# Kernel optimization log

Measured on AMD Instinct MI355X. Metric: run time of the kernel, lower is better.

## Reference

```python
import jax, jax.numpy as jnp
import numpy as np

B, T, D, E, K = 8, 4096, 1024, 64, 2


def setup_inputs() -> dict:
    key = jax.random.key(0)
    k1, k2, k3, k4 = jax.random.split(key, 4)
    return {
        "mh_output": jax.random.normal(k1, (B, T, D), dtype=jnp.float32),
        "W_route": jax.random.normal(k2, (D, E), dtype=jnp.float32) * (1.0 / np.sqrt(D)),
        "b_route": jnp.zeros((E,), dtype=jnp.float32),
        "W_noise": jax.random.normal(k3, (D, E), dtype=jnp.float32) * (1.0 / np.sqrt(D)),
        "b_noise": jnp.zeros((E,), dtype=jnp.float32),
        "noise_u": jax.random.uniform(k4, (B, T, E), dtype=jnp.float32),
        "top_k": K,
    }


def reference(mh_output, W_route, b_route, W_noise, b_noise, noise_u, top_k):
    # [B,T,D] @ [D,E] -> [B,T,E]
    logits = jnp.einsum("btd,de->bte", mh_output, W_route) + b_route
    noise_logits = jnp.einsum("btd,de->bte", mh_output, W_noise) + b_noise
    noisy_logits = logits + noise_u * jax.nn.softplus(noise_logits)
    # top-k over experts
    top_k_logits, indices = jax.lax.top_k(noisy_logits, top_k)  # [B,T,K]
    # scatter top-k values back into -inf canvas == mask non-topk to -inf
    mask = jax.nn.one_hot(indices, E, dtype=jnp.bool_).any(axis=-2)  # [B,T,E]
    sparse_logits = jnp.where(mask, noisy_logits, -jnp.inf)
    router_output = jax.nn.softmax(sparse_logits, axis=-1)
    return (router_output, indices)
```

## Files before the change

### kernel.cpp

```cpp
#include <hip/hip_runtime.h>
#include <math.h>

#define MROWS 32768
#define DDIM  1024
#define EDIM  64
#define NCH   64
#define TILEM 64

typedef _Float16 f16x8 __attribute__((ext_vector_type(8)));
typedef float    f32x16 __attribute__((ext_vector_type(16)));

__global__ __launch_bounds__(256)
void convW_kernel(const float* __restrict__ Wr, const float* __restrict__ Wn,
                  unsigned short* __restrict__ ws) {
    int gid = blockIdx.x * 256 + threadIdx.x;
    int c32 = gid & 31;
    int j   = (gid >> 5) & 7;
    int lhi = (gid >> 8) & 1;
    int nf  = (gid >> 9) & 3;
    int c   = gid >> 11;
    int lane = lhi * 32 + c32;
    int k   = c * 16 + lhi * 8 + j;
    int col = nf * 32 + c32;
    float w = (col < EDIM) ? Wr[k * EDIM + col] : Wn[k * EDIM + (col - EDIM)];
    _Float16 hi = (_Float16)w;
    _Float16 lo = (_Float16)((w - (float)hi) * 2048.0f);
    union { _Float16 h; unsigned short u; } cv;
    size_t base = (size_t)c * 4096 + nf * 512 + lane * 8 + j;
    cv.h = hi; ws[base]        = cv.u;
    cv.h = lo; ws[base + 2048] = cv.u;
}

__global__ __launch_bounds__(256)
void router_mfma(const float* __restrict__ X,
                 const unsigned short* __restrict__ WS,
                 const float* __restrict__ br_g,
                 const float* __restrict__ bn_g,
                 const float* __restrict__ U,
                 float* __restrict__ out)
{
    __shared__ alignas(16) unsigned char smem[32768];
    unsigned short* Ah = (unsigned short*)smem;
    unsigned short* Bh = (unsigned short*)(smem + 12288);
    float*          Lf = (float*)smem;

    const int t    = threadIdx.x;
    const int lane = t & 63;
    const int wid  = t >> 6;
    const int wm   = wid >> 1;
    const int wn   = wid & 1;
    const int rowBase = blockIdx.x * TILEM;

    f32x16 acc0[2], acc1[2];
#pragma unroll
    for (int n = 0; n < 2; ++n)
#pragma unroll
        for (int i = 0; i < 16; ++i) { acc0[n][i] = 0.f; acc1[n][i] = 0.f; }

    const int arow = t >> 2;
    const int ak0  = (t & 3) * 4;
    const float* xsrc = X + (size_t)(rowBase + arow) * DDIM + ak0;

    auto convA = [&](float4 x, int buf) {
        union { _Float16 h[4]; uint2 v; } H, L;
        float xs[4] = {x.x, x.y, x.z, x.w};
#pragma unroll
        for (int i = 0; i < 4; ++i) {
            _Float16 hi = (_Float16)xs[i];
            H.h[i] = hi;
            L.h[i] = (_Float16)((xs[i] - (float)hi) * 2048.0f);
        }
        *(uint2*)(Ah + ((buf * 2 + 0) * 64 + arow) * 24 + ak0) = H.v;
        *(uint2*)(Ah + ((buf * 2 + 1) * 64 + arow) * 24 + ak0) = L.v;
    };

    auto compute = [&](int buf) {
        const unsigned short* Ab = Ah + (buf * 2) * 1536;
        const int aoff = (wm * 32 + (lane & 31)) * 24 + ((lane >> 5) * 8);
        f16x8 ahi = *(const f16x8*)(Ab + aoff);
        f16x8 alo = *(const f16x8*)(Ab + 1536 + aoff);
        const unsigned short* Bb = Bh + buf * 4096;
#pragma unroll
        for (int nfl = 0; nfl < 2; ++nfl) {
            const int nfg = wn * 2 + nfl;
            f16x8 bhi = *(const f16x8*)(Bb + nfg * 512 + lane * 8);
            f16x8 blo = *(const f16x8*)(Bb + 2048 + nfg * 512 + lane * 8);
            acc0[nfl] = __builtin_amdgcn_mfma_f32_32x32x16_f16(ahi, bhi, acc0[nfl], 0, 0, 0);
            acc1[nfl] = __builtin_amdgcn_mfma_f32_32x32x16_f16(ahi, blo, acc1[nfl], 0, 0, 0);
            acc1[nfl] = __builtin_amdgcn_mfma_f32_32x32x16_f16(alo, bhi, acc1[nfl], 0, 0, 0);
        }
    };

    float4 x0 = *(const float4*)(xsrc);
    {
        uint4 b0 = *(const uint4*)(WS + t * 16);
        uint4 b1 = *(const uint4*)(WS + t * 16 + 8);
        convA(x0, 0);
        *(uint4*)(Bh + t * 16)     = b0;
        *(uint4*)(Bh + t * 16 + 8) = b1;
    }
    float4 xN = *(const float4*)(xsrc + 1 * 16);
    float4 xF = *(const float4*)(xsrc + 2 * 16);
    __syncthreads();

#define ITER(C, BUF, XN_, XF_)                                                 \
    {                                                                          \
        uint4 b0{}, b1{};                                                      \
        if ((C) + 1 < NCH) {                                                   \
            const unsigned short* wp = WS + (size_t)((C) + 1) * 4096 + t * 16; \
            b0 = *(const uint4*)(wp);                                          \
            b1 = *(const uint4*)(wp + 8);                                      \
        }                                                                      \
        compute(BUF);                                                          \
        if ((C) + 1 < NCH) {                                                   \
            convA(XN_, (BUF) ^ 1);                                             \
            *(uint4*)(Bh + ((BUF) ^ 1) * 4096 + t * 16)     = b0;              \
            *(uint4*)(Bh + ((BUF) ^ 1) * 4096 + t * 16 + 8) = b1;              \
        }                                                                      \
        if ((C) + 3 < NCH) XN_ = *(const float4*)(xsrc + ((C) + 3) * 16);      \
        __syncthreads();                                                       \
    }

    for (int c = 0; c < NCH; c += 2) {
        ITER(c,     0, xN, xF);
        ITER(c + 1, 1, xF, xN);
    }
#undef ITER

    const float inv2048 = 1.0f / 2048.0f;
#pragma unroll
    for (int nfl = 0; nfl < 2; ++nfl) {
#pragma unroll
        for (int reg = 0; reg < 16; ++reg) {
            float v = acc0[nfl][reg] + acc1[nfl][reg] * inv2048;
            int rl  = (reg & 3) + ((reg >> 2) << 3) + ((lane >> 5) << 2);
            int row = wm * 32 + rl;
            int col = wn * 64 + nfl * 32 + (lane & 31);
            Lf[row * 128 + col] = v;
        }
    }
    __syncthreads();

    const float brv = br_g[lane];
    const float bnv = bn_g[lane];
#pragma unroll 4
    for (int r = 0; r < 16; ++r) {
        int row  = wid * 16 + r;
        int grow = rowBase + row;
        float lr = Lf[row * 128 + lane] + brv;
        float ln = Lf[row * 128 + 64 + lane] + bnv;
        float u  = U[(size_t)grow * EDIM + lane];
        float noisy = lr + u * log1pf(expf(ln));

        float m1 = noisy; int i1 = lane;
        float m2 = -INFINITY; int i2 = 64;
#pragma unroll
        for (int s = 1; s < 64; s <<= 1) {
            float om1 = __shfl_xor(m1, s);
            int   oi1 = __shfl_xor(i1, s);
            float om2 = __shfl_xor(m2, s);
            int   oi2 = __shfl_xor(i2, s);
            bool aw = (m1 > om1) || (m1 == om1 && i1 < oi1);
            float w1  = aw ? m1 : om1;  int wi1  = aw ? i1 : oi1;
            float c2a = aw ? m2 : om2;  int c2ai = aw ? i2 : oi2;
            float c2b = aw ? om1 : m1;  int c2bi = aw ? oi1 : i1;
            bool bw = (c2b > c2a) || (c2b == c2a && c2bi < c2ai);
            m1 = w1; i1 = wi1;
            m2 = bw ? c2b : c2a;
            i2 = bw ? c2bi : c2ai;
        }
        float e2  = expf(m2 - m1);
        float inv = 1.0f / (1.0f + e2);
        float p   = (lane == i1) ? inv : ((lane == i2) ? e2 * inv : 0.0f);
        out[(size_t)grow * EDIM + lane] = p;
        if (lane < 2)
            out[(size_t)MROWS * EDIM + (size_t)grow * 2 + lane] =
                (float)(lane == 0 ? i1 : i2);
    }
}

extern "C" void kernel_launch(void* const* d_in, const int* in_sizes, int n_in,
                              void* d_out, int out_size, void* d_ws, size_t ws_size,
                              hipStream_t stream) {
    const float* X  = (const float*)d_in[0];
    const float* Wr = (const float*)d_in[1];
    const float* br = (const float*)d_in[2];
    const float* Wn = (const float*)d_in[3];
    const float* bn = (const float*)d_in[4];
    const float* U  = (const float*)d_in[5];
    (void)in_sizes; (void)n_in; (void)ws_size;
    unsigned short* ws16 = (unsigned short*)d_ws;
    convW_kernel<<<512, 256, 0, stream>>>(Wr, Wn, ws16);
    router_mfma<<<MROWS / TILEM, 256, 0, stream>>>(X, ws16, br, bn, U, (float*)d_out);
}
```

Before: 64.11 us.

## Load X directly into registers per wave and stage W via global_load_lds

Each wave now owns 32 rows and all 128 output columns. X is read straight from global memory into MFMA operand registers, so the LDS staging of A is gone. W chunks are copied asynchronously into LDS with global_load_lds, and the tile grows to 128 rows per block. The epilogue runs top-2 and softmax directly on the accumulator registers with a 32-lane reduction, which removes the LDS round trip for the logits. The cost is more accumulator registers (occupancy pinned at one block per SM) and uncoalesced per-lane X loads.

```diff
diff --git a/kernel.cpp b/kernel.cpp
--- a/kernel.cpp
+++ b/kernel.cpp
@@ -5,7 +5,7 @@
 #define DDIM  1024
 #define EDIM  64
 #define NCH   64
-#define TILEM 64
+#define TILEM 128
 
 typedef _Float16 f16x8 __attribute__((ext_vector_type(8)));
 typedef float    f32x16 __attribute__((ext_vector_type(16)));
@@ -31,7 +31,7 @@
     cv.h = lo; ws[base + 2048] = cv.u;
 }
 
-__global__ __launch_bounds__(256)
+__global__ __launch_bounds__(256, 1)
 void router_mfma(const float* __restrict__ X,
                  const unsigned short* __restrict__ WS,
                  const float* __restrict__ br_g,
@@ -39,127 +39,113 @@
                  const float* __restrict__ U,
                  float* __restrict__ out)
 {
-    __shared__ alignas(16) unsigned char smem[32768];
-    unsigned short* Ah = (unsigned short*)smem;
-    unsigned short* Bh = (unsigned short*)(smem + 12288);
-    float*          Lf = (float*)smem;
+    __shared__ unsigned short Bh[2][4096];
 
     const int t    = threadIdx.x;
     const int lane = t & 63;
-    const int wid  = t >> 6;
-    const int wm   = wid >> 1;
-    const int wn   = wid & 1;
+    const int wid  = __builtin_amdgcn_readfirstlane(t >> 6);
     const int rowBase = blockIdx.x * TILEM;
+    const int myRow = rowBase + wid * 32 + (lane & 31);
+    const int kSub  = (lane >> 5) * 8;
+    const float* xp = X + (size_t)myRow * DDIM + kSub;
+    const char* wsB = (const char*)WS;
 
-    f32x16 acc0[2], acc1[2];
+    f32x16 acc0[4], acc1[4];
 #pragma unroll
-    for (int n = 0; n < 2; ++n)
+    for (int nf = 0; nf < 4; ++nf)
 #pragma unroll
-        for (int i = 0; i < 16; ++i) { acc0[n][i] = 0.f; acc1[n][i] = 0.f; }
+        for (int i = 0; i < 16; ++i) { acc0[nf][i] = 0.f; acc1[nf][i] = 0.f; }
 
-    const int arow = t >> 2;
-    const int ak0  = (t & 3) * 4;
-    const float* xsrc = X + (size_t)(rowBase + arow) * DDIM + ak0;
-
-    auto convA = [&](float4 x, int buf) {
-        union { _Float16 h[4]; uint2 v; } H, L;
-        float xs[4] = {x.x, x.y, x.z, x.w};
+    auto stageB = [&](int c, int buf) {
 #pragma unroll
-        for (int i = 0; i < 4; ++i) {
-            _Float16 hi = (_Float16)xs[i];
-            H.h[i] = hi;
-            L.h[i] = (_Float16)((xs[i] - (float)hi) * 2048.0f);
-        }
-        *(uint2*)(Ah + ((buf * 2 + 0) * 64 + arow) * 24 + ak0) = H.v;
-        *(uint2*)(Ah + ((buf * 2 + 1) * 64 + arow) * 24 + ak0) = L.v;
-    };
-
-    auto compute = [&](int buf) {
-        const unsigned short* Ab = Ah + (buf * 2) * 1536;
-        const int aoff = (wm * 32 + (lane & 31)) * 24 + ((lane >> 5) * 8);
-        f16x8 ahi = *(const f16x8*)(Ab + aoff);
-        f16x8 alo = *(const f16x8*)(Ab + 1536 + aoff);
-        const unsigned short* Bb = Bh + buf * 4096;
-#pragma unroll
-        for (int nfl = 0; nfl < 2; ++nfl) {
-            const int nfg = wn * 2 + nfl;
-            f16x8 bhi = *(const f16x8*)(Bb + nfg * 512 + lane * 8);
-            f16x8 blo = *(const f16x8*)(Bb + 2048 + nfg * 512 + lane * 8);
-            acc0[nfl] = __builtin_amdgcn_mfma_f32_32x32x16_f16(ahi, bhi, acc0[nfl], 0, 0, 0);
-            acc1[nfl] = __builtin_amdgcn_mfma_f32_32x32x16_f16(ahi, blo, acc1[nfl], 0, 0, 0);
-            acc1[nfl] = __builtin_amdgcn_mfma_f32_32x32x16_f16(alo, bhi, acc1[nfl], 0, 0, 0);
+        for (int r = 0; r < 2; ++r) {
+            int o = r * 4096 + wid * 1024;
+            __builtin_amdgcn_global_load_lds(
+                (const __attribute__((address_space(1))) void*)(wsB + (size_t)c * 8192 + o + lane * 16),
+                (__attribute__((address_space(3))) void*)((char*)&Bh[buf][0] + o),
+                16, 0, 0);
         }
     };
 
-    float4 x0 = *(const float4*)(xsrc);
-    {
-        uint4 b0 = *(const uint4*)(WS + t * 16);
-        uint4 b1 = *(const uint4*)(WS + t * 16 + 8);
-        convA(x0, 0);
-        *(uint4*)(Bh + t * 16)     = b0;
-        *(uint4*)(Bh + t * 16 + 8) = b1;
-    }
-    float4 xN = *(const float4*)(xsrc + 1 * 16);
-    float4 xF = *(const float4*)(xsrc + 2 * 16);
+    auto convA8 = [&](const float4& a, const float4& b, f16x8& hi, f16x8& lo) {
+        float x[8] = {a.x, a.y, a.z, a.w, b.x, b.y, b.z, b.w};
+#pragma unroll
+        for (int j = 0; j < 8; ++j) {
+            _Float16 h = (_Float16)x[j];
+            hi[j] = h;
+            lo[j] = (_Float16)((x[j] - (float)h) * 2048.0f);
+        }
+    };
+
+    auto compute = [&](int buf, const f16x8& ahi, const f16x8& alo) {
+        const unsigned short* Bb = &Bh[buf][0];
+#pragma unroll
+        for (int nf = 0; nf < 4; ++nf) {
+            f16x8 bhi = *(const f16x8*)(Bb + nf * 512 + lane * 8);
+            f16x8 blo = *(const f16x8*)(Bb + 2048 + nf * 512 + lane * 8);
+            acc0[nf] = __builtin_amdgcn_mfma_f32_32x32x16_f16(ahi, bhi, acc0[nf], 0, 0, 0);
+            acc1[nf] = __builtin_amdgcn_mfma_f32_32x32x16_f16(ahi, blo, acc1[nf], 0, 0, 0);
+            acc1[nf] = __builtin_amdgcn_mfma_f32_32x32x16_f16(alo, bhi, acc1[nf], 0, 0, 0);
+        }
+    };
+
+    stageB(0, 0);
+    float4 xA0 = *(const float4*)(xp);
+    float4 xA1 = *(const float4*)(xp + 4);
+    float4 xB0 = *(const float4*)(xp + 16);
+    float4 xB1 = *(const float4*)(xp + 20);
     __syncthreads();
 
-#define ITER(C, BUF, XN_, XF_)                                                 \
-    {                                                                          \
-        uint4 b0{}, b1{};                                                      \
-        if ((C) + 1 < NCH) {                                                   \
-            const unsigned short* wp = WS + (size_t)((C) + 1) * 4096 + t * 16; \
-            b0 = *(const uint4*)(wp);                                          \
-            b1 = *(const uint4*)(wp + 8);                                      \
-        }                                                                      \
-        compute(BUF);                                                          \
-        if ((C) + 1 < NCH) {                                                   \
-            convA(XN_, (BUF) ^ 1);                                             \
-            *(uint4*)(Bh + ((BUF) ^ 1) * 4096 + t * 16)     = b0;              \
-            *(uint4*)(Bh + ((BUF) ^ 1) * 4096 + t * 16 + 8) = b1;              \
-        }                                                                      \
-        if ((C) + 3 < NCH) XN_ = *(const float4*)(xsrc + ((C) + 3) * 16);      \
-        __syncthreads();                                                       \
+    for (int c = 0; c < NCH; c += 2) {
+        if (c + 1 < NCH) stageB(c + 1, 1);
+        {
+            f16x8 ahi, alo;
+            convA8(xA0, xA1, ahi, alo);
+            if (c + 2 < NCH) {
+                xA0 = *(const float4*)(xp + (c + 2) * 16);
+                xA1 = *(const float4*)(xp + (c + 2) * 16 + 4);
+            }
+            compute(0, ahi, alo);
+        }
+        __syncthreads();
+        if (c + 2 < NCH) stageB(c + 2, 0);
+        {
+            f16x8 ahi, alo;
+            convA8(xB0, xB1, ahi, alo);
+            if (c + 3 < NCH) {
+                xB0 = *(const float4*)(xp + (c + 3) * 16);
+                xB1 = *(const float4*)(xp + (c + 3) * 16 + 4);
+            }
+            compute(1, ahi, alo);
+        }
+        __syncthreads();
     }
 
-    for (int c = 0; c < NCH; c += 2) {
-        ITER(c,     0, xN, xF);
-        ITER(c + 1, 1, xF, xN);
-    }
-#undef ITER
+    const int c0 = lane & 31;
+    const float br0 = br_g[c0],      br1 = br_g[32 + c0];
+    const float bn0 = bn_g[c0],      bn1 = bn_g[32 + c0];
+    const int rBase2 = rowBase + wid * 32 + 4 * (lane >> 5);
+    const float inv2048 = 1.0f / 2048.0f;
 
-    const float inv2048 = 1.0f / 2048.0f;
 #pragma unroll
-    for (int nfl = 0; nfl < 2; ++nfl) {
+    for (int reg = 0; reg < 16; ++reg) {
+        int grow = rBase2 + (reg & 3) + 8 * (reg >> 2);
+        float v0 = acc0[0][reg] + acc1[0][reg] * inv2048;
+        float v1 = acc0[1][reg] + acc1[1][reg] * inv2048;
+        float v2 = acc0[2][reg] + acc1[2][reg] * inv2048;
+        float v3 = acc0[3][reg] + acc1[3][reg] * inv2048;
+        float u0 = U[(size_t)grow * EDIM + c0];
+        float u1 = U[(size_t)grow * EDIM + 32 + c0];
+        float n0 = (v0 + br0) + u0 * log1pf(expf(v2 + bn0));
+        float n1 = (v1 + br1) + u1 * log1pf(expf(v3 + bn1));
+
+        float m1, m2; int i1, i2;
+        if (n0 >= n1) { m1 = n0; i1 = c0;      m2 = n1; i2 = 32 + c0; }
+        else          { m1 = n1; i1 = 32 + c0; m2 = n0; i2 = c0;      }
 #pragma unroll
-        for (int reg = 0; reg < 16; ++reg) {
-            float v = acc0[nfl][reg] + acc1[nfl][reg] * inv2048;
-            int rl  = (reg & 3) + ((reg >> 2) << 3) + ((lane >> 5) << 2);
-            int row = wm * 32 + rl;
-            int col = wn * 64 + nfl * 32 + (lane & 31);
-            Lf[row * 128 + col] = v;
-        }
-    }
-    __syncthreads();
-
-    const float brv = br_g[lane];
-    const float bnv = bn_g[lane];
-#pragma unroll 4
-    for (int r = 0; r < 16; ++r) {
-        int row  = wid * 16 + r;
-        int grow = rowBase + row;
-        float lr = Lf[row * 128 + lane] + brv;
-        float ln = Lf[row * 128 + 64 + lane] + bnv;
-        float u  = U[(size_t)grow * EDIM + lane];
-        float noisy = lr + u * log1pf(expf(ln));
-
-        float m1 = noisy; int i1 = lane;
-        float m2 = -INFINITY; int i2 = 64;
-#pragma unroll
-        for (int s = 1; s < 64; s <<= 1) {
-            float om1 = __shfl_xor(m1, s);
-            int   oi1 = __shfl_xor(i1, s);
-            float om2 = __shfl_xor(m2, s);
-            int   oi2 = __shfl_xor(i2, s);
+        for (int s = 1; s < 32; s <<= 1) {
+            float om1 = __shfl_xor(m1, s); int oi1 = __shfl_xor(i1, s);
+            float om2 = __shfl_xor(m2, s); int oi2 = __shfl_xor(i2, s);
             bool aw = (m1 > om1) || (m1 == om1 && i1 < oi1);
             float w1  = aw ? m1 : om1;  int wi1  = aw ? i1 : oi1;
             float c2a = aw ? m2 : om2;  int c2ai = aw ? i2 : oi2;
@@ -171,11 +157,14 @@
         }
         float e2  = expf(m2 - m1);
         float inv = 1.0f / (1.0f + e2);
-        float p   = (lane == i1) ? inv : ((lane == i2) ? e2 * inv : 0.0f);
-        out[(size_t)grow * EDIM + lane] = p;
-        if (lane < 2)
-            out[(size_t)MROWS * EDIM + (size_t)grow * 2 + lane] =
-                (float)(lane == 0 ? i1 : i2);
+        float P1 = inv, P2 = e2 * inv;
+        float p0 = (i1 == c0)      ? P1 : ((i2 == c0)      ? P2 : 0.0f);
+        float p1 = (i1 == 32 + c0) ? P1 : ((i2 == 32 + c0) ? P2 : 0.0f);
+        out[(size_t)grow * EDIM + c0]      = p0;
+        out[(size_t)grow * EDIM + 32 + c0] = p1;
+        if (c0 < 2)
+            out[(size_t)MROWS * EDIM + (size_t)grow * 2 + c0] =
+                (float)(c0 == 0 ? i1 : i2);
     }
 }
 
```

Result: slower. 80.91 us (+26.2%).
